# Kernel tuning notes

Measured on AMD Instinct MI355X. Metric: run time of the kernel, lower is better.

## Reference

```python
import jax, jax.numpy as jnp
import numpy as np

D_K = 128
D_V = 128
SEQ_LEN = 2048


def setup_inputs() -> dict:
    key = jax.random.key(0)
    kq, kk, kv = jax.random.split(key, 3)
    q = jax.random.normal(kq, (SEQ_LEN, D_K), dtype=jnp.float32)
    k = jax.random.normal(kk, (SEQ_LEN, D_K), dtype=jnp.float32)
    v = jax.random.normal(kv, (SEQ_LEN, D_V), dtype=jnp.float32)
    return {"q": q, "k": k, "v": v}


def _step(carry, qkv):
    J, Svv, Sqv, Sqq, l = carry
    q, k, v = qkv
    l = l + 1
    fl = l.astype(J.dtype)
    # update_correlations: running means of outer products
    Svv = (fl - 1.0) / fl * Svv + jnp.outer(v, v) / fl
    Sqv = (fl - 1.0) / fl * Sqv + jnp.outer(q, v) / fl
    Sqq = (fl - 1.0) / fl * Sqq + jnp.outer(q, q) / fl

    first = l == 1

    # ecological params (J: [d_v, d_k], Sqv: [d_k, d_v], Sqq: [d_k, d_k])
    s_J = jnp.einsum('vk,kv->', J, Sqv)            # trace(J @ Sigma_qv)
    s_l = k @ Sqv @ v
    A_JJ = jnp.einsum('vk,kj,vj->', J, Sqq, J)     # trace(J Sqq J^T)
    A_ll = (v @ v) * (k @ Sqq @ k)
    A_Jl = v @ J @ Sqq @ k

    # safe denominators (unused branches must not produce NaN under where)
    A_JJ_s = jnp.where(first | (A_JJ == 0), 1.0, A_JJ)
    A_ll_s = jnp.where(first | (A_ll == 0), 1.0, A_ll)
    denom = A_JJ * A_ll - A_Jl ** 2
    denom_s = jnp.where(first | (denom == 0), 1.0, denom)

    margin = s_l - A_Jl * (s_J / A_JJ_s)

    wf = (A_ll * s_J - A_Jl * s_l) / denom_s
    wi = (A_JJ * s_l - A_Jl * s_J) / denom_s
    # nonnegativity constraints (check omega_i first, as in the source)
    wf_c = jnp.where(wi <= 0, s_J / A_JJ_s, jnp.where(wf <= 0, 0.0, wf))
    wi_c = jnp.where(wi <= 0, 0.0, jnp.where(wf <= 0, s_l / A_ll_s, wi))

    do_update = margin > 0
    vk = jnp.outer(v, k)
    J_upd = jnp.where(do_update, wf_c * J + wi_c * vk, J)
    J_new = jnp.where(first, vk, J_upd)
    updated = first | do_update

    # compute_cost with updated J and correlations
    cost = (0.5 * jnp.trace(Svv)
            - jnp.einsum('vk,kv->', J_new, Sqv)
            + 0.5 * jnp.einsum('vk,kj,vj->', J_new, Sqq, J_new))

    return (J_new, Svv, Sqv, Sqq, l), (cost, updated)


def _run(q, k, v):
    d_k, d_v = q.shape[-1], v.shape[-1]
    init = (jnp.zeros((d_v, d_k), q.dtype),
            jnp.zeros((d_v, d_v), q.dtype),
            jnp.zeros((d_k, d_v), q.dtype),
            jnp.zeros((d_k, d_k), q.dtype),
            jnp.int32(0))
    (J, _, _, _, _), (costs, updated) = jax.lax.scan(_step, init, (q, k, v))
    return costs, updated, J


def reference(q, k, v):
    return _run(q, k, v)
```

## Files before the change

kernel.cpp:

```cpp
#include <hip/hip_runtime.h>

#define SEQ 2048
#define D 128

typedef float v2f __attribute__((ext_vector_type(2)));
typedef float v4f __attribute__((ext_vector_type(4)));
#define LO2(v) __builtin_shufflevector(v, v, 0, 1)
#define HI2(v) __builtin_shufflevector(v, v, 2, 3)

#define DPP_ADD(x, ctrl) \
    ((x) + __int_as_float(__builtin_amdgcn_update_dpp(0, __float_as_int(x), (ctrl), 0xf, 0xf, true)))
#define COMBINE8(x) do { x = DPP_ADD(x, 0xB1); x = DPP_ADD(x, 0x4E); x = DPP_ADD(x, 0x141); } while (0)
#define TAIL3(x)    do { x = DPP_ADD(x, 0x140); x = DPP_ADD(x, 0x142); x = DPP_ADD(x, 0x143); } while (0)
#define REDUCE16(x) do { x = DPP_ADD(x, 0xB1); x = DPP_ADD(x, 0x4E); x = DPP_ADD(x, 0x141); \
                         x = DPP_ADD(x, 0x140); } while (0)

#define UPDATE_J(MODE, WF, WI)                                                \
    if ((MODE) == 2) {                                                        \
        const v2f vc2 = {vcur, vcur};                                         \
        j0 = vc2 * k0_; j1 = vc2 * k1_; j2 = vc2 * k2_; j3 = vc2 * k3_;       \
        j4 = vc2 * k4_; j5 = vc2 * k5_; j6 = vc2 * k6_; j7 = vc2 * k7_;       \
    } else if ((MODE) == 1) {                                                 \
        const v2f wf2 = {(WF), (WF)};                                         \
        const float wvr_ = (WI) * vcur;                                       \
        const v2f wv2 = {wvr_, wvr_};                                         \
        j0 = __builtin_elementwise_fma(j0, wf2, wv2 * k0_);                   \
        j1 = __builtin_elementwise_fma(j1, wf2, wv2 * k1_);                   \
        j2 = __builtin_elementwise_fma(j2, wf2, wv2 * k2_);                   \
        j3 = __builtin_elementwise_fma(j3, wf2, wv2 * k3_);                   \
        j4 = __builtin_elementwise_fma(j4, wf2, wv2 * k4_);                   \
        j5 = __builtin_elementwise_fma(j5, wf2, wv2 * k5_);                   \
        j6 = __builtin_elementwise_fma(j6, wf2, wv2 * k6_);                   \
        j7 = __builtin_elementwise_fma(j7, wf2, wv2 * k7_);                   \
    }

__global__ __launch_bounds__(1024, 4) void fused_kernel(
    const float* __restrict__ q, const float* __restrict__ k, const float* __restrict__ v,
    float* __restrict__ U, float* __restrict__ sl_arr,
    float* __restrict__ kqq_arr, float* __restrict__ vv_arr,
    float* __restrict__ kq_adj, float* __restrict__ vv_adj,
    float* __restrict__ kU_adj, double* __restrict__ invl_arr,
    float* __restrict__ out, int* flags)
{
    const int tid  = threadIdx.x;
    const int lane = tid & 63;

    __shared__ double lpad[8448];
    if (tid == 0) lpad[0] = (double)blockIdx.x;

    if (blockIdx.x != 0) {
        const int b = blockIdx.x - 1;

        __shared__ float ks[D];
        __shared__ float vs[D];
        __shared__ float alpha[SEQ];
        __shared__ float red[32];
        __shared__ float upart[1024];

        for (int rr = 0; rr < 8; ++rr) {
            const int s = b * 8 + rr;
            __syncthreads();

            if (tid < D) ks[tid] = k[s * D + tid];
            else if (tid < 2 * D) vs[tid - D] = v[s * D + (tid - D)];
            __syncthreads();

            float p_a2 = 0.f, p_ab = 0.f;
            for (int i = tid; i <= s; i += 1024) {
                const float4* qr = (const float4*)(q + (size_t)i * D);
                const float4* vr = (const float4*)(v + (size_t)i * D);
                float a = 0.f, bb = 0.f;
#pragma unroll
                for (int j = 0; j < D / 4; ++j) {
                    float4 q4 = qr[j];
                    float4 v4 = vr[j];
                    a += q4.x * ks[4 * j + 0] + q4.y * ks[4 * j + 1] + q4.z * ks[4 * j + 2] + q4.w * ks[4 * j + 3];
                    bb += v4.x * vs[4 * j + 0] + v4.y * vs[4 * j + 1] + v4.z * vs[4 * j + 2] + v4.w * vs[4 * j + 3];
                }
                alpha[i] = a;
                p_a2 += a * a;
                p_ab += a * bb;
                if (i == s) vv_arr[s] = bb;
            }
#pragma unroll
            for (int off = 1; off < 64; off <<= 1) {
                p_a2 += __shfl_xor(p_a2, off);
                p_ab += __shfl_xor(p_ab, off);
            }
            const int wid = tid >> 6;
            if ((tid & 63) == 0) { red[wid] = p_a2; red[16 + wid] = p_ab; }
            __syncthreads();
            if (tid == 0) {
                float s1 = 0.f, s2 = 0.f;
#pragma unroll
                for (int j = 0; j < 16; ++j) { s1 += red[j]; s2 += red[16 + j]; }
                kqq_arr[s] = s1;
                sl_arr[s]  = s2;
                invl_arr[s] = 1.0 / (double)(s + 1);
            }

            if (tid < 64) {
                if (s + 1 < SEQ) {
                    float p2 = ks[tid] * q[(size_t)(s + 1) * D + tid]
                             + ks[tid + 64] * q[(size_t)(s + 1) * D + 64 + tid];
#pragma unroll
                    for (int off = 1; off < 64; off <<= 1) p2 += __shfl_xor(p2, off);
                    if (tid == 0) kq_adj[s + 1] = p2;
                }
                if (s == 0 && tid == 0) { kq_adj[0] = 0.f; kU_adj[0] = 0.f; vv_adj[0] = 0.f; }
            } else if (tid < 128 && s > 0) {
                const int t2 = tid - 64;
                float p2 = vs[t2] * v[(size_t)(s - 1) * D + t2]
                         + vs[t2 + 64] * v[(size_t)(s - 1) * D + 64 + t2];
#pragma unroll
                for (int off = 1; off < 64; off <<= 1) p2 += __shfl_xor(p2, off);
                if (t2 == 0) vv_adj[s] = p2;
            }

            const int c = tid & (D - 1);
            const int h = tid >> 7;
            float a0 = 0.f, a1 = 0.f, a2 = 0.f, a3 = 0.f;
            int i = h;
            for (; i + 24 <= s; i += 32) {
                a0 = fmaf(q[(size_t)(i     ) * D + c], alpha[i     ], a0);
                a1 = fmaf(q[(size_t)(i +  8) * D + c], alpha[i +  8], a1);
                a2 = fmaf(q[(size_t)(i + 16) * D + c], alpha[i + 16], a2);
                a3 = fmaf(q[(size_t)(i + 24) * D + c], alpha[i + 24], a3);
            }
            for (; i <= s; i += 8) a0 = fmaf(q[(size_t)i * D + c], alpha[i], a0);
            upart[tid] = (a0 + a1) + (a2 + a3);
            __syncthreads();

            float kup = 0.f;
            if (tid < D) {
                float uv = 0.f;
#pragma unroll
                for (int j = 0; j < 8; ++j) uv += upart[tid + 128 * j];
                U[(size_t)s * D + tid] = uv;
                if (s > 0) kup = uv * k[(size_t)(s - 1) * D + tid];
            }
#pragma unroll
            for (int off = 1; off < 64; off <<= 1) kup += __shfl_xor(kup, off);
            if (tid == 0)  red[0] = kup;
            if (tid == 64) red[1] = kup;
            __syncthreads();
            if (s > 0 && tid == 0) kU_adj[s] = red[0] + red[1];
        }

        __syncthreads();
        __threadfence();
        if (tid == 0)
            __hip_atomic_store(&flags[b], 1, __ATOMIC_RELEASE, __HIP_MEMORY_SCOPE_AGENT);
        return;
    }

#define WAITGATE(T)                                                           \
    {                                                                         \
        int t_ = (T); if (t_ > SEQ - 1) t_ = SEQ - 1;                         \
        const int fb_ = t_ >> 3;                      \
        for (;;) {                                                            \
            int ok_ = 1;                                                      \
            _Pragma("unroll")                                                 \
            for (int jj_ = 0; jj_ < 4; ++jj_) {                               \
                const int fi_ = lane + 64 * jj_;                              \
                if (fi_ <= fb_)                                               \
                    ok_ &= __hip_atomic_load(&flags[fi_],                     \
                             __ATOMIC_ACQUIRE, __HIP_MEMORY_SCOPE_AGENT);     \
            }                                                                 \
            if (__all(ok_)) break;                                            \
            __builtin_amdgcn_s_sleep(8);                                      \
        }                                                                     \
    }

    const int w    = __builtin_amdgcn_readfirstlane(tid >> 6);
    const int r    = tid >> 3;
    const int cg   = tid & 7;
    const int c0s  = cg * 20;

    v2f j0 = {0.f, 0.f}, j1 = j0, j2 = j0, j3 = j0, j4 = j0, j5 = j0, j6 = j0, j7 = j0;

    __shared__ float ring[3][3][160];
    __shared__ __align__(16) float wred[3][16][4];
    __shared__ __align__(16) float decLDS[3][4];

    const bool stager = (tid >= 384) && (tid < 768);
    const int  which  = (tid >> 7) - 3;
    const int  sidx   = tid & 127;
    const int  widx   = ((sidx >> 4) * 20) + (sidx & 15);

    WAITGATE(99)

    float gstage = 0.f;
    if (stager) {
        if (which == 0) {
            ring[0][0][widx] = q[(size_t)1 * D + sidx];
            ring[1][0][widx] = q[(size_t)2 * D + sidx];
            gstage = q[(size_t)3 * D + sidx];
        } else if (which == 1) {
            ring[0][1][widx] = U[(size_t)1 * D + sidx];
            ring[1][1][widx] = U[(size_t)2 * D + sidx];
            gstage = U[(size_t)3 * D + sidx];
        } else {
            ring[0][2][widx] = k[sidx];
            ring[1][2][widx] = k[(size_t)1 * D + sidx];
            gstage = k[(size_t)2 * D + sidx];
        }
    }
    float vcur = v[r], vnext = v[(size_t)D + r], vn2 = v[(size_t)2 * D + r];

    float dwf = 0.f, dwi = 1.f;
    int dmode = 2;
    if (tid == 0) { decLDS[0][0] = 0.f; decLDS[0][1] = 1.f; decLDS[0][2] = 2.f; decLDS[0][3] = 0.f; }

    double SJ = 0.0, AJJ = 0.0, trSvv = 0.0;
    if (w == 0) {
        const double sl0 = (double)sl_arr[0];
        const double kq0 = (double)kqq_arr[0];
        const double vv0 = (double)vv_arr[0];
        trSvv = vv0;
        SJ  = sl0;
        AJJ = vv0 * kq0;
        if (lane == 0) {
            out[0] = (float)((0.5 * trSvv - SJ + 0.5 * AJJ) * invl_arr[0]);
            out[SEQ] = 1.f;
        }
    }
    __syncthreads();

#define STEP_BODY(I, P, PN, PW)                                               \
{                                                                             \
    float c_sl = 0.f, c_kq = 0.f, c_vv = 0.f, c_kqa = 0.f, c_vva = 0.f,       \
          c_vvp = 0.f, c_kua = 0.f;                                           \
    double c_inv = 0.0;                                                       \
    if (w == 0) {                                                             \
        c_sl  = sl_arr[(I) + 1];  c_kq  = kqq_arr[(I) + 1];                   \
        c_vv  = vv_arr[(I) + 1];  c_kqa = kq_adj[(I) + 1];                    \
        c_vva = vv_adj[(I) + 1];  c_vvp = vv_arr[(I)];                        \
        c_kua = kU_adj[(I) + 1];  c_inv = invl_arr[(I) + 1];                  \
    }                                                                         \
    const v4f Qa = ((const v4f*)&ring[P][0][c0s])[0];                         \
    const v4f Qb = ((const v4f*)&ring[P][0][c0s])[1];                         \
    const v4f Qc = ((const v4f*)&ring[P][0][c0s])[2];                         \
    const v4f Qd = ((const v4f*)&ring[P][0][c0s])[3];                         \
    const v4f Ua = ((const v4f*)&ring[P][1][c0s])[0];                         \
    const v4f Ub = ((const v4f*)&ring[P][1][c0s])[1];                         \
    const v4f Uc = ((const v4f*)&ring[P][1][c0s])[2];                         \
    const v4f Ud = ((const v4f*)&ring[P][1][c0s])[3];                         \
    const v4f Ka = ((const v4f*)&ring[P][2][c0s])[0];                         \
    const v4f Kb = ((const v4f*)&ring[P][2][c0s])[1];                         \
    const v4f Kc = ((const v4f*)&ring[P][2][c0s])[2];                         \
    const v4f Kd = ((const v4f*)&ring[P][2][c0s])[3];                         \
    const v2f k0_ = LO2(Ka), k1_ = HI2(Ka), k2_ = LO2(Kb), k3_ = HI2(Kb);     \
    const v2f k4_ = LO2(Kc), k5_ = HI2(Kc), k6_ = LO2(Kd), k7_ = HI2(Kd);     \
    v2f aq0 = {0.f, 0.f}, aq1 = aq0, aq2 = aq0, aq3 = aq0;                    \
    aq0 = __builtin_elementwise_fma(j0, LO2(Qa), aq0);                        \
    aq1 = __builtin_elementwise_fma(j1, HI2(Qa), aq1);                        \
    aq2 = __builtin_elementwise_fma(j2, LO2(Qb), aq2);                        \
    aq3 = __builtin_elementwise_fma(j3, HI2(Qb), aq3);                        \
    aq0 = __builtin_elementwise_fma(j4, LO2(Qc), aq0);                        \
    aq1 = __builtin_elementwise_fma(j5, HI2(Qc), aq1);                        \
    aq2 = __builtin_elementwise_fma(j6, LO2(Qd), aq2);                        \
    aq3 = __builtin_elementwise_fma(j7, HI2(Qd), aq3);                        \
    const v2f sq_ = (aq0 + aq1) + (aq2 + aq3);                                \
    float Yq = sq_.x + sq_.y;                                                 \
    v2f au0 = {0.f, 0.f}, au1 = au0, au2 = au0, au3 = au0;                    \
    au0 = __builtin_elementwise_fma(j0, LO2(Ua), au0);                        \
    au1 = __builtin_elementwise_fma(j1, HI2(Ua), au1);                        \
    au2 = __builtin_elementwise_fma(j2, LO2(Ub), au2);                        \
    au3 = __builtin_elementwise_fma(j3, HI2(Ub), au3);                        \
    au0 = __builtin_elementwise_fma(j4, LO2(Uc), au0);                        \
    au1 = __builtin_elementwise_fma(j5, HI2(Uc), au1);                        \
    au2 = __builtin_elementwise_fma(j6, LO2(Ud), au2);                        \
    au3 = __builtin_elementwise_fma(j7, HI2(Ud), au3);                        \
    const v2f su_ = (au0 + au1) + (au2 + au3);                                \
    float Yw = su_.x + su_.y;                                                 \
    COMBINE8(Yq);                                                             \
    COMBINE8(Yw);                                                             \
    float z1 = vnext * Yq;                                                    \
    float z2 = Yq * Yq;                                                       \
    float z3 = vcur  * Yq;                                                    \
    float z4 = vnext * Yw;                                                    \
    TAIL3(z1);                                                                \
    TAIL3(z2);                                                                \
    TAIL3(z3);                                                                \
    TAIL3(z4);                                                                \
    if (lane == 63) *(float4*)&wred[P][w][0] = make_float4(z1, z2, z3, z4);   \
    __syncthreads();                                                          \
    if (stager) {                                                             \
        ring[PW][which][widx] = gstage;                                       \
        const int tq_ = ((I) + 4 < SEQ) ? (I) + 4 : SEQ - 1;                  \
        const int tk_ = ((I) + 3 < SEQ) ? (I) + 3 : SEQ - 1;                  \
        gstage = (which == 0) ? q[(size_t)tq_ * D + sidx]                     \
               : (which == 1) ? U[(size_t)tq_ * D + sidx]                     \
                              : k[(size_t)tk_ * D + sidx];                    \
    }                                                                         \
    const int tv_ = ((I) + 3 < SEQ) ? (I) + 3 : SEQ - 1;                      \
    const float vnew_ = v[(size_t)tv_ * D + r];                               \
    if (w == 0) {                                                             \
        float4 ww = *(const float4*)&wred[P][lane & 15][0];                   \
        const float odwf = dwf, odwi = dwi;                                   \
        const int   odmode = dmode;                                           \
        UPDATE_J(odmode, odwf, odwi)                                          \
        REDUCE16(ww.x);                                                       \
        REDUCE16(ww.y);                                                       \
        REDUCE16(ww.z);                                                       \
        REDUCE16(ww.w);                                                       \
        double a_, b_;                                                        \
        if (odmode == 2)      { a_ = 0.0; b_ = 1.0; }                         \
        else if (odmode == 1) { a_ = (double)odwf; b_ = (double)odwi; }       \
        else                  { a_ = 1.0; b_ = 0.0; }                         \
        const double kqa = (double)c_kqa, vva = (double)c_vva;                \
        const double vvp = (double)c_vvp, kua = (double)c_kua;                \
        const double r1 = (double)ww.x * 0.125, r2 = (double)ww.y * 0.125;    \
        const double r3 = (double)ww.z * 0.125, r4 = (double)ww.w * 0.125;    \
        const double Jqv  = a_ * r1 + b_ * (kqa * vva);                       \
        const double Jq2  = a_ * a_ * r2 + 2.0 * a_ * b_ * kqa * r3          \
                          + b_ * b_ * kqa * kqa * vvp;                        \
        const double AJl_ = a_ * r4 + b_ * kua * vva;                         \
        trSvv += (double)c_vv;                                                \
        SJ    += Jqv;                                                         \
        AJJ   += Jq2;                                                         \
        const double s_l  = (double)c_sl;                                     \
        const double A_ll = (double)c_vv * (double)c_kq;                      \
        const double AJJ_s  = (AJJ == 0.0)  ? 1.0 : AJJ;                      \
        const double A_ll_s = (A_ll == 0.0) ? 1.0 : A_ll;                     \
        const double denom   = AJJ * A_ll - AJl_ * AJl_;                      \
        const double denom_s = (denom == 0.0) ? 1.0 : denom;                  \
        const double rden = 1.0 / denom_s;                                    \
        const double wf = (A_ll * SJ - AJl_ * s_l) * rden;                    \
        const double wi = (AJJ * s_l - AJl_ * SJ) * rden;                     \
        double wf_c, wi_c;                                                    \
        if (wi <= 0.0)      { wf_c = SJ / AJJ_s;  wi_c = 0.0; }               \
        else if (wf <= 0.0) { wf_c = 0.0;         wi_c = s_l / A_ll_s; }      \
        else                { wf_c = wf;          wi_c = wi; }                \
        const bool do_update = (s_l * AJJ_s - AJl_ * SJ) > 0.0;               \
        int mode;                                                             \
        if (do_update) {                                                      \
            mode = 1;                                                         \
            const double nSJ = wf_c * SJ + wi_c * s_l;                        \
            AJJ = wf_c * wf_c * AJJ + 2.0 * wf_c * wi_c * AJl_                \
                + wi_c * wi_c * A_ll;                                         \
            SJ = nSJ;                                                         \
        } else {                                                              \
            mode = 0;                                                         \
        }                                                                     \
        dwf = (float)wf_c; dwi = (float)wi_c; dmode = mode;                   \
        if (lane == 0) {                                                      \
            out[(I) + 1] = (float)((0.5 * trSvv - SJ + 0.5 * AJJ) * c_inv);   \
            out[SEQ + (I) + 1] = mode ? 1.f : 0.f;                            \
            *(float4*)&decLDS[PN][0] = make_float4(dwf, dwi, (float)mode, 0.f);\
        }                                                                     \
    } else {                                                                  \
        const float4 df = *(const float4*)&decLDS[P][0];                      \
        dwf = df.x; dwi = df.y; dmode = (int)df.z;                            \
        UPDATE_J(dmode, dwf, dwi)                                             \
    }                                                                         \
    vcur = vnext; vnext = vn2; vn2 = vnew_;                                   \
}

    for (int i = 0; i + 2 < SEQ - 1; i += 3) {
        if (i && (i % 96) == 0) WAITGATE(i + 99)
        STEP_BODY(i,     0, 1, 2)
        STEP_BODY(i + 1, 1, 2, 0)
        STEP_BODY(i + 2, 2, 0, 1)
    }
    STEP_BODY(SEQ - 2, 0, 1, 2)
#undef STEP_BODY
#undef WAITGATE

    __syncthreads();
    {
        const float4 df = *(const float4*)&decLDS[1][0];
        const float fwf = df.x, fwi = df.y;
        const int   fmode = (int)df.z;
        const v4f Ka = ((const v4f*)&ring[1][2][c0s])[0];
        const v4f Kb = ((const v4f*)&ring[1][2][c0s])[1];
        const v4f Kc = ((const v4f*)&ring[1][2][c0s])[2];
        const v4f Kd = ((const v4f*)&ring[1][2][c0s])[3];
        const v2f k0_ = LO2(Ka), k1_ = HI2(Ka), k2_ = LO2(Kb), k3_ = HI2(Kb);
        const v2f k4_ = LO2(Kc), k5_ = HI2(Kc), k6_ = LO2(Kd), k7_ = HI2(Kd);
        UPDATE_J(fmode, fwf, fwi)
        float* jbase = out + 2 * SEQ + (size_t)r * D + cg * 16;
        *(v4f*)(jbase + 0)  = __builtin_shufflevector(j0, j1, 0, 1, 2, 3);
        *(v4f*)(jbase + 4)  = __builtin_shufflevector(j2, j3, 0, 1, 2, 3);
        *(v4f*)(jbase + 8)  = __builtin_shufflevector(j4, j5, 0, 1, 2, 3);
        *(v4f*)(jbase + 12) = __builtin_shufflevector(j6, j7, 0, 1, 2, 3);
    }
}

extern "C" void kernel_launch(void* const* d_in, const int* in_sizes, int n_in,
                              void* d_out, int out_size, void* d_ws, size_t ws_size,
                              hipStream_t stream) {
    (void)in_sizes; (void)n_in; (void)out_size; (void)ws_size;
    const float* q = (const float*)d_in[0];
    const float* k = (const float*)d_in[1];
    const float* v = (const float*)d_in[2];
    float* out = (float*)d_out;

    float* U      = (float*)d_ws;
    float* sl     = U + (size_t)SEQ * D;
    float* kqq    = sl + SEQ;
    float* vv     = kqq + SEQ;
    float* kq_adj = vv + SEQ;
    float* vv_adj = kq_adj + SEQ;
    float* kU_adj = vv_adj + SEQ;
    double* invl  = (double*)(kU_adj + SEQ);
    int*    flags = (int*)(invl + SEQ);

    hipMemsetAsync(flags, 0, 256 * sizeof(int), stream);
    fused_kernel<<<257, 1024, 0, stream>>>(q, k, v, U, sl, kqq, vv,
                                           kq_adj, vv_adj, kU_adj, invl,
                                           out, flags);
}
```

Before: 2.549 ms.

## Split producer blocks into four concurrent 256-thread rows per block

Producer blocks now handle 4 sequence rows at a time, one per 256-thread group, in parallel rather than 8 rows sequentially per 1024-thread block. The grid doubles to 513 blocks and the consumer's flag wait is adjusted to match. The lpad shared-memory padding array, which looks like it was there to limit occupancy, is removed, and the launch bounds change from 4 to 2. The goal is to produce the precomputed U, alpha and scalar terms faster so the serial consumer block waits less, at the cost of more blocks and more shared memory for the 4 alpha arrays.

```diff
diff --git a/kernel.cpp b/kernel.cpp
--- a/kernel.cpp
+++ b/kernel.cpp
@@ -34,7 +34,7 @@
         j7 = __builtin_elementwise_fma(j7, wf2, wv2 * k7_);                   \
     }
 
-__global__ __launch_bounds__(1024, 4) void fused_kernel(
+__global__ __launch_bounds__(1024, 2) void fused_kernel(
     const float* __restrict__ q, const float* __restrict__ k, const float* __restrict__ v,
     float* __restrict__ U, float* __restrict__ sl_arr,
     float* __restrict__ kqq_arr, float* __restrict__ vv_arr,
@@ -45,107 +45,97 @@
     const int tid  = threadIdx.x;
     const int lane = tid & 63;
 
-    __shared__ double lpad[8448];
-    if (tid == 0) lpad[0] = (double)blockIdx.x;
-
     if (blockIdx.x != 0) {
         const int b = blockIdx.x - 1;
-
-        __shared__ float ks[D];
-        __shared__ float vs[D];
-        __shared__ float alpha[SEQ];
-        __shared__ float red[32];
-        __shared__ float upart[1024];
-
-        for (int rr = 0; rr < 8; ++rr) {
-            const int s = b * 8 + rr;
-            __syncthreads();
-
-            if (tid < D) ks[tid] = k[s * D + tid];
-            else if (tid < 2 * D) vs[tid - D] = v[s * D + (tid - D)];
-            __syncthreads();
-
-            float p_a2 = 0.f, p_ab = 0.f;
-            for (int i = tid; i <= s; i += 1024) {
-                const float4* qr = (const float4*)(q + (size_t)i * D);
-                const float4* vr = (const float4*)(v + (size_t)i * D);
-                float a = 0.f, bb = 0.f;
+        const int g = tid >> 8;
+        const int t = tid & 255;
+        const int s = b * 4 + g;
+
+        __shared__ float ks[4][D];
+        __shared__ float vs[4][D];
+        __shared__ float alpha[4][SEQ];
+        __shared__ float red[4][8];
+        __shared__ float upart[4][256];
+
+        if (t < D) ks[g][t] = k[s * D + t];
+        else vs[g][t - D] = v[s * D + (t - D)];
+        __syncthreads();
+
+        float p_a2 = 0.f, p_ab = 0.f;
+        for (int i = t; i <= s; i += 256) {
+            const float4* qr = (const float4*)(q + (size_t)i * D);
+            const float4* vr = (const float4*)(v + (size_t)i * D);
+            float a = 0.f, bb = 0.f;
 #pragma unroll
-                for (int j = 0; j < D / 4; ++j) {
-                    float4 q4 = qr[j];
-                    float4 v4 = vr[j];
-                    a += q4.x * ks[4 * j + 0] + q4.y * ks[4 * j + 1] + q4.z * ks[4 * j + 2] + q4.w * ks[4 * j + 3];
-                    bb += v4.x * vs[4 * j + 0] + v4.y * vs[4 * j + 1] + v4.z * vs[4 * j + 2] + v4.w * vs[4 * j + 3];
-                }
-                alpha[i] = a;
-                p_a2 += a * a;
-                p_ab += a * bb;
-                if (i == s) vv_arr[s] = bb;
+            for (int j = 0; j < D / 4; ++j) {
+                float4 q4 = qr[j];
+                float4 v4 = vr[j];
+                a += q4.x * ks[g][4 * j + 0] + q4.y * ks[g][4 * j + 1] + q4.z * ks[g][4 * j + 2] + q4.w * ks[g][4 * j + 3];
+                bb += v4.x * vs[g][4 * j + 0] + v4.y * vs[g][4 * j + 1] + v4.z * vs[g][4 * j + 2] + v4.w * vs[g][4 * j + 3];
             }
+            alpha[g][i] = a;
+            p_a2 += a * a;
+            p_ab += a * bb;
+            if (i == s) vv_arr[s] = bb;
+        }
 #pragma unroll
-            for (int off = 1; off < 64; off <<= 1) {
-                p_a2 += __shfl_xor(p_a2, off);
-                p_ab += __shfl_xor(p_ab, off);
-            }
-            const int wid = tid >> 6;
-            if ((tid & 63) == 0) { red[wid] = p_a2; red[16 + wid] = p_ab; }
-            __syncthreads();
-            if (tid == 0) {
-                float s1 = 0.f, s2 = 0.f;
-#pragma unroll
-                for (int j = 0; j < 16; ++j) { s1 += red[j]; s2 += red[16 + j]; }
-                kqq_arr[s] = s1;
-                sl_arr[s]  = s2;
-                invl_arr[s] = 1.0 / (double)(s + 1);
-            }
-
-            if (tid < 64) {
-                if (s + 1 < SEQ) {
-                    float p2 = ks[tid] * q[(size_t)(s + 1) * D + tid]
-                             + ks[tid + 64] * q[(size_t)(s + 1) * D + 64 + tid];
-#pragma unroll
-                    for (int off = 1; off < 64; off <<= 1) p2 += __shfl_xor(p2, off);
-                    if (tid == 0) kq_adj[s + 1] = p2;
-                }
-                if (s == 0 && tid == 0) { kq_adj[0] = 0.f; kU_adj[0] = 0.f; vv_adj[0] = 0.f; }
-            } else if (tid < 128 && s > 0) {
-                const int t2 = tid - 64;
-                float p2 = vs[t2] * v[(size_t)(s - 1) * D + t2]
-                         + vs[t2 + 64] * v[(size_t)(s - 1) * D + 64 + t2];
+        for (int off = 1; off < 64; off <<= 1) {
+            p_a2 += __shfl_xor(p_a2, off);
+            p_ab += __shfl_xor(p_ab, off);
+        }
+        const int wid = t >> 6;
+        if ((t & 63) == 0) { red[g][wid] = p_a2; red[g][4 + wid] = p_ab; }
+        __syncthreads();
+        if (t == 0) {
+            kqq_arr[s] = red[g][0] + red[g][1] + red[g][2] + red[g][3];
+            sl_arr[s]  = red[g][4] + red[g][5] + red[g][6] + red[g][7];
+            invl_arr[s] = 1.0 / (double)(s + 1);
+        }
+
+        if (t < 64) {
+            if (s + 1 < SEQ) {
+                float p2 = ks[g][t] * q[(size_t)(s + 1) * D + t]
+                         + ks[g][t + 64] * q[(size_t)(s + 1) * D + 64 + t];
 #pragma unroll
                 for (int off = 1; off < 64; off <<= 1) p2 += __shfl_xor(p2, off);
-                if (t2 == 0) vv_adj[s] = p2;
+                if (t == 0) kq_adj[s + 1] = p2;
             }
-
-            const int c = tid & (D - 1);
-            const int h = tid >> 7;
-            float a0 = 0.f, a1 = 0.f, a2 = 0.f, a3 = 0.f;
-            int i = h;
-            for (; i + 24 <= s; i += 32) {
-                a0 = fmaf(q[(size_t)(i     ) * D + c], alpha[i     ], a0);
-                a1 = fmaf(q[(size_t)(i +  8) * D + c], alpha[i +  8], a1);
-                a2 = fmaf(q[(size_t)(i + 16) * D + c], alpha[i + 16], a2);
-                a3 = fmaf(q[(size_t)(i + 24) * D + c], alpha[i + 24], a3);
-            }
-            for (; i <= s; i += 8) a0 = fmaf(q[(size_t)i * D + c], alpha[i], a0);
-            upart[tid] = (a0 + a1) + (a2 + a3);
-            __syncthreads();
-
-            float kup = 0.f;
-            if (tid < D) {
-                float uv = 0.f;
+            if (s == 0 && t == 0) { kq_adj[0] = 0.f; kU_adj[0] = 0.f; vv_adj[0] = 0.f; }
+        } else if (t < 128 && s > 0) {
+            const int t2 = t - 64;
+            float p2 = vs[g][t2] * v[(size_t)(s - 1) * D + t2]
+                     + vs[g][t2 + 64] * v[(size_t)(s - 1) * D + 64 + t2];
 #pragma unroll
-                for (int j = 0; j < 8; ++j) uv += upart[tid + 128 * j];
-                U[(size_t)s * D + tid] = uv;
-                if (s > 0) kup = uv * k[(size_t)(s - 1) * D + tid];
-            }
+            for (int off = 1; off < 64; off <<= 1) p2 += __shfl_xor(p2, off);
+            if (t2 == 0) vv_adj[s] = p2;
+        }
+
+        const int c = t & (D - 1);
+        const int h = t >> 7;
+        float a0 = 0.f, a1 = 0.f, a2 = 0.f, a3 = 0.f;
+        int i = h;
+        for (; i + 6 <= s; i += 8) {
+            a0 = fmaf(q[(size_t)(i    ) * D + c], alpha[g][i    ], a0);
+            a1 = fmaf(q[(size_t)(i + 2) * D + c], alpha[g][i + 2], a1);
+            a2 = fmaf(q[(size_t)(i + 4) * D + c], alpha[g][i + 4], a2);
+            a3 = fmaf(q[(size_t)(i + 6) * D + c], alpha[g][i + 6], a3);
+        }
+        for (; i <= s; i += 2) a0 = fmaf(q[(size_t)i * D + c], alpha[g][i], a0);
+        upart[g][t] = (a0 + a1) + (a2 + a3);
+        __syncthreads();
+
+        float kup = 0.f;
+        if (t < D) {
+            const float uv = upart[g][t] + upart[g][t + D];
+            U[(size_t)s * D + t] = uv;
+            if (s > 0) kup = uv * k[(size_t)(s - 1) * D + t];
+        }
 #pragma unroll
-            for (int off = 1; off < 64; off <<= 1) kup += __shfl_xor(kup, off);
-            if (tid == 0)  red[0] = kup;
-            if (tid == 64) red[1] = kup;
-            __syncthreads();
-            if (s > 0 && tid == 0) kU_adj[s] = red[0] + red[1];
-        }
+        for (int off = 1; off < 64; off <<= 1) kup += __shfl_xor(kup, off);
+        if (t == 0)  red[g][0] = kup;
+        if (t == 64) red[g][1] = kup;
+        __syncthreads();
+        if (s > 0 && t == 0) kU_adj[s] = red[g][0] + red[g][1];
 
         __syncthreads();
         __threadfence();
@@ -157,11 +147,11 @@
 #define WAITGATE(T)                                                           \
     {                                                                         \
         int t_ = (T); if (t_ > SEQ - 1) t_ = SEQ - 1;                         \
-        const int fb_ = t_ >> 3;                      \
+        const int fb_ = t_ >> 2;                      \
         for (;;) {                                                            \
             int ok_ = 1;                                                      \
             _Pragma("unroll")                                                 \
-            for (int jj_ = 0; jj_ < 4; ++jj_) {                               \
+            for (int jj_ = 0; jj_ < 8; ++jj_) {                               \
                 const int fi_ = lane + 64 * jj_;                              \
                 if (fi_ <= fb_)                                               \
                     ok_ &= __hip_atomic_load(&flags[fi_],                     \
@@ -407,8 +397,8 @@
     double* invl  = (double*)(kU_adj + SEQ);
     int*    flags = (int*)(invl + SEQ);
 
-    hipMemsetAsync(flags, 0, 256 * sizeof(int), stream);
-    fused_kernel<<<257, 1024, 0, stream>>>(q, k, v, U, sl, kqq, vv,
+    hipMemsetAsync(flags, 0, 512 * sizeof(int), stream);
+    fused_kernel<<<513, 1024, 0, stream>>>(q, k, v, U, sl, kqq, vv,
                                            kq_adj, vv_adj, kU_adj, invl,
                                            out, flags);
 }
```

Result: no change. 2.597 ms (+1.9%).
